# Kernel tuning notes

Hardware: AMD Instinct MI355X
Metric: run time of the kernel (lower is better)

Reference implementation:

```python
import jax, jax.numpy as jnp
import numpy as np


def setup_inputs() -> dict:
    key = jax.random.key(0)
    k1, k2 = jax.random.split(key)
    B, N, C = 2, 1024, 64  # batch_size, block_num, out_channels
    regional_means = jax.random.normal(k1, (B, N, C), dtype=jnp.float32)
    # nn.Parameter randn then kaiming_uniform_: just use scaled random weights
    W = jax.random.normal(k2, (C, C), dtype=jnp.float32) * (1.0 / np.sqrt(C))
    return {"regional_means": regional_means, "W": W, "c": C}


def reference(regional_means, W, c):
    # regional_means: (B, N, c); W: (c, c)
    B, N, _ = regional_means.shape
    M = W @ W.T  # (c, c), PSD Mahalanobis metric
    # pairwise differences diff[b, i, j] = means[b, i] - means[b, j]  -> (B, N, N, c)
    # (original materializes this via repeat/permute; sign flip from its final
    #  permute is irrelevant since the quadratic form is even)
    diff = regional_means[:, :, None, :] - regional_means[:, None, :, :]
    # quadratic form q[b,i,j] = diff^T M diff
    q = jnp.einsum('bijc,cd,bijd->bij', diff, M, diff)
    adj = jnp.exp(-q) + jnp.eye(N, dtype=regional_means.dtype)[None, :, :]
    return adj
```

## Files before the change

### kernel.cpp

```cpp
#include <hip/hip_runtime.h>
#include <hip/hip_bf16.h>
#include <math.h>


typedef __attribute__((ext_vector_type(8))) short bf16x8;
typedef __attribute__((ext_vector_type(4))) float f32x4;

#define PITCH 72

static __device__ __forceinline__ void store4bf(__hip_bfloat16* p, float4 v) {
    __hip_bfloat16 h[4] = {__float2bfloat16(v.x), __float2bfloat16(v.y),
                           __float2bfloat16(v.z), __float2bfloat16(v.w)};
    *(uint2*)p = *(const uint2*)h;
}

__global__ void __launch_bounds__(512, 4) adj_fused_mfma2(
    const float* __restrict__ X, const float* __restrict__ W,
    float* __restrict__ out, int N)
{
    __shared__ __hip_bfloat16 sX[2][64][PITCH];
    __shared__ __hip_bfloat16 sWT[64][PITCH];
    __shared__ float rs[2][64];

    const int b    = blockIdx.z;
    const int ib   = blockIdx.y << 6;
    const int jb   = blockIdx.x << 6;
    const bool diag = (ib == jb);
    const int t    = threadIdx.x;
    const int w    = t >> 6;
    const int lane = t & 63;
    const int m    = lane & 15;
    const int q    = lane >> 4;

    const float* __restrict__ Xb = X + (size_t)b * N * 64;

    const float4* W4  = (const float4*)W;
    const float4* Xi4 = (const float4*)(Xb + (size_t)ib * 64);
    const float4* Xj4 = (const float4*)(Xb + (size_t)jb * 64);
#pragma unroll
    for (int it = 0; it < 2; ++it) {
        const int idx = it * 512 + t;
        const int row = idx >> 4;
        const int c4  = (idx & 15) << 2;
        const float4 wv = W4[idx];
        sWT[c4 + 0][row] = __float2bfloat16(wv.x);
        sWT[c4 + 1][row] = __float2bfloat16(wv.y);
        sWT[c4 + 2][row] = __float2bfloat16(wv.z);
        sWT[c4 + 3][row] = __float2bfloat16(wv.w);
        store4bf(&sX[0][row][c4], Xi4[idx]);
        if (!diag) store4bf(&sX[1][row][c4], Xj4[idx]);
    }
    __syncthreads();

    {
        const int src  = w >> 2;
        const int band = (w & 3) << 4;
        if (!(diag && src)) {
            const bf16x8 a0 = *(const bf16x8*)&sX[src][band + m][q * 8];
            const bf16x8 a1 = *(const bf16x8*)&sX[src][band + m][q * 8 + 32];
            float p[4] = {0.f, 0.f, 0.f, 0.f};
#pragma unroll
            for (int ci = 0; ci < 4; ++ci) {
                const bf16x8 b0 = *(const bf16x8*)&sWT[(ci << 4) + m][q * 8];
                const bf16x8 b1 = *(const bf16x8*)&sWT[(ci << 4) + m][q * 8 + 32];
                f32x4 acc = {0.f, 0.f, 0.f, 0.f};
                acc = __builtin_amdgcn_mfma_f32_16x16x32_bf16(a0, b0, acc, 0, 0, 0);
                acc = __builtin_amdgcn_mfma_f32_16x16x32_bf16(a1, b1, acc, 0, 0, 0);
#pragma unroll
                for (int v = 0; v < 4; ++v) {
                    const __hip_bfloat16 hb = __float2bfloat16(acc[v]);
                    sX[src][band + q * 4 + v][(ci << 4) + m] = hb;
                    const float f = __bfloat162float(hb);
                    p[v] = fmaf(f, f, p[v]);
                }
            }
#pragma unroll
            for (int off = 1; off < 16; off <<= 1)
#pragma unroll
                for (int v = 0; v < 4; ++v) p[v] += __shfl_xor(p[v], off, 64);
            if (m == 0)
#pragma unroll
                for (int v = 0; v < 4; ++v) rs[src][band + q * 4 + v] = p[v];
        }
    }
    __syncthreads();

    const __hip_bfloat16 (*pYi)[PITCH] = sX[0];
    const __hip_bfloat16 (*pYj)[PITCH] = diag ? sX[0] : sX[1];
    const float* prj = diag ? rs[0] : rs[1];

    const int jband = (w & 3) << 4;
    const int ihalf = w >> 2;

    const bf16x8 ja0 = *(const bf16x8*)&pYj[jband + m][q * 8];
    const bf16x8 ja1 = *(const bf16x8*)&pYj[jband + m][q * 8 + 32];
    float rj[4];
#pragma unroll
    for (int v = 0; v < 4; ++v) rj[v] = prj[jband + (q << 2) + v];

    const size_t obase = (size_t)b * N * N;
#pragma unroll
    for (int s = 0; s < 2; ++s) {
        const int isub   = (ihalf << 1) + s;
        const int ilocal = (isub << 4) + m;
        const bf16x8 ib0 = *(const bf16x8*)&pYi[ilocal][q * 8];
        const bf16x8 ib1 = *(const bf16x8*)&pYi[ilocal][q * 8 + 32];
        f32x4 acc = {0.f, 0.f, 0.f, 0.f};
        acc = __builtin_amdgcn_mfma_f32_16x16x32_bf16(ja0, ib0, acc, 0, 0, 0);
        acc = __builtin_amdgcn_mfma_f32_16x16x32_bf16(ja1, ib1, acc, 0, 0, 0);
        const float riv = rs[0][ilocal];
        f32x4 vals;
#pragma unroll
        for (int v = 0; v < 4; ++v) {
            const float qq = riv + rj[v] - 2.f * acc[v];
            float val = __expf(-qq);
            if (diag && ilocal == jband + (q << 2) + v) val += 1.f;
            vals[v] = val;
        }
        *(f32x4*)&out[obase + (size_t)(ib + ilocal) * N + jb + jband + (q << 2)]
            = vals;
    }
}

extern "C" void kernel_launch(void* const* d_in, const int* in_sizes, int n_in,
                              void* d_out, int out_size, void* d_ws, size_t ws_size,
                              hipStream_t stream) {
    (void)n_in; (void)d_ws; (void)ws_size;
    const float* X = (const float*)d_in[0];
    const float* W = (const float*)d_in[1];
    float* out = (float*)d_out;

    const int C  = 64;
    const int BN = in_sizes[0] / C;
    const int N  = (int)(((long long)out_size * C) / in_sizes[0]);
    const int B  = BN / N;

    adj_fused_mfma2<<<dim3(N / 64, N / 64, B), 512, 0, stream>>>(X, W, out, N);
}
```

Baseline: 63.26 us.

## Precompute Y=XW and row norms once in workspace, then run gram-only kernel

Splits the fused kernel into two launches. The first computes Y = X·W (bf16) and the squared row norms once per row and writes them to the workspace buffer. The second reads Y directly from global memory to build the Gram tile and apply the exp. This removes the redundant per-tile recomputation of X·W and the shared-memory staging, at the cost of an extra launch and a dependency between the two kernels. The fused kernel remains as a fallback when the workspace is missing or too small.

```diff
diff --git a/kernel.cpp b/kernel.cpp
--- a/kernel.cpp
+++ b/kernel.cpp
@@ -12,6 +12,110 @@
     __hip_bfloat16 h[4] = {__float2bfloat16(v.x), __float2bfloat16(v.y),
                            __float2bfloat16(v.z), __float2bfloat16(v.w)};
     *(uint2*)p = *(const uint2*)h;
+}
+
+__global__ void __launch_bounds__(256, 2) compute_y(
+    const float* __restrict__ X, const float* __restrict__ W,
+    __hip_bfloat16* __restrict__ Yw, float* __restrict__ Rw)
+{
+    __shared__ __hip_bfloat16 sX[64][PITCH];
+    __shared__ __hip_bfloat16 sWT[64][PITCH];
+    const int t    = threadIdx.x;
+    const int wv   = t >> 6;
+    const int lane = t & 63;
+    const int m    = lane & 15;
+    const int q    = lane >> 4;
+    const int band = wv << 4;
+    const long long r0 = (long long)blockIdx.x << 6;
+
+    const float4* W4 = (const float4*)W;
+    const float4* X4 = (const float4*)(X + r0 * 64);
+#pragma unroll
+    for (int it = 0; it < 4; ++it) {
+        const int idx = it * 256 + t;
+        const int row = idx >> 4;
+        const int c4  = (idx & 15) << 2;
+        const float4 wv4 = W4[idx];
+        sWT[c4 + 0][row] = __float2bfloat16(wv4.x);
+        sWT[c4 + 1][row] = __float2bfloat16(wv4.y);
+        sWT[c4 + 2][row] = __float2bfloat16(wv4.z);
+        sWT[c4 + 3][row] = __float2bfloat16(wv4.w);
+        store4bf(&sX[row][c4], X4[idx]);
+    }
+    __syncthreads();
+
+    const bf16x8 a0 = *(const bf16x8*)&sX[band + m][q * 8];
+    const bf16x8 a1 = *(const bf16x8*)&sX[band + m][q * 8 + 32];
+    float p[4] = {0.f, 0.f, 0.f, 0.f};
+#pragma unroll
+    for (int ci = 0; ci < 4; ++ci) {
+        const bf16x8 b0 = *(const bf16x8*)&sWT[(ci << 4) + m][q * 8];
+        const bf16x8 b1 = *(const bf16x8*)&sWT[(ci << 4) + m][q * 8 + 32];
+        f32x4 acc = {0.f, 0.f, 0.f, 0.f};
+        acc = __builtin_amdgcn_mfma_f32_16x16x32_bf16(a0, b0, acc, 0, 0, 0);
+        acc = __builtin_amdgcn_mfma_f32_16x16x32_bf16(a1, b1, acc, 0, 0, 0);
+#pragma unroll
+        for (int v = 0; v < 4; ++v) {
+            const __hip_bfloat16 hb = __float2bfloat16(acc[v]);
+            Yw[(r0 + band + q * 4 + v) * 64 + (ci << 4) + m] = hb;
+            const float f = __bfloat162float(hb);
+            p[v] = fmaf(f, f, p[v]);
+        }
+    }
+#pragma unroll
+    for (int off = 1; off < 16; off <<= 1)
+#pragma unroll
+        for (int v = 0; v < 4; ++v) p[v] += __shfl_xor(p[v], off, 64);
+    if (m == 0)
+#pragma unroll
+        for (int v = 0; v < 4; ++v) Rw[r0 + band + q * 4 + v] = p[v];
+}
+
+__global__ void __launch_bounds__(512, 4) adj_gram(
+    const __hip_bfloat16* __restrict__ Yw, const float* __restrict__ Rw,
+    float* __restrict__ out, int N)
+{
+    const int b     = blockIdx.z;
+    const int ibase = blockIdx.y << 6;
+    const int jbase = blockIdx.x << 6;
+    const int t     = threadIdx.x;
+    const int w     = t >> 6;
+    const int lane  = t & 63;
+    const int m     = lane & 15;
+    const int q     = lane >> 4;
+    const int jband = (w & 3) << 4;
+    const int ihalf = w >> 2;
+
+    const __hip_bfloat16* __restrict__ Yb = Yw + (size_t)b * N * 64;
+    const float* __restrict__ Rb = Rw + (size_t)b * N;
+
+    const int jrow = jbase + jband + m;
+    const bf16x8 ja0 = *(const bf16x8*)&Yb[(size_t)jrow * 64 + q * 8];
+    const bf16x8 ja1 = *(const bf16x8*)&Yb[(size_t)jrow * 64 + q * 8 + 32];
+    const f32x4 rj = *(const f32x4*)&Rb[jbase + jband + (q << 2)];
+
+    const size_t obase = (size_t)b * N * N;
+#pragma unroll
+    for (int s = 0; s < 2; ++s) {
+        const int ilocal = (((ihalf << 1) + s) << 4) + m;
+        const int irow   = ibase + ilocal;
+        const bf16x8 ib0 = *(const bf16x8*)&Yb[(size_t)irow * 64 + q * 8];
+        const bf16x8 ib1 = *(const bf16x8*)&Yb[(size_t)irow * 64 + q * 8 + 32];
+        f32x4 acc = {0.f, 0.f, 0.f, 0.f};
+        acc = __builtin_amdgcn_mfma_f32_16x16x32_bf16(ja0, ib0, acc, 0, 0, 0);
+        acc = __builtin_amdgcn_mfma_f32_16x16x32_bf16(ja1, ib1, acc, 0, 0, 0);
+        const float riv  = Rb[irow];
+        const int jcol0  = jbase + jband + (q << 2);
+        f32x4 vals;
+#pragma unroll
+        for (int v = 0; v < 4; ++v) {
+            const float qq = fmaf(-2.f, acc[v], riv + rj[v]);
+            float val = __expf(-qq);
+            if (irow == jcol0 + v) val += 1.f;
+            vals[v] = val;
+        }
+        *(f32x4*)&out[obase + (size_t)irow * N + jcol0] = vals;
+    }
 }
 
 __global__ void __launch_bounds__(512, 4) adj_fused_mfma2(
@@ -33,7 +137,6 @@
     const int q    = lane >> 4;
 
     const float* __restrict__ Xb = X + (size_t)b * N * 64;
-
     const float4* W4  = (const float4*)W;
     const float4* Xi4 = (const float4*)(Xb + (size_t)ib * 64);
     const float4* Xj4 = (const float4*)(Xb + (size_t)jb * 64);
@@ -125,7 +228,7 @@
 extern "C" void kernel_launch(void* const* d_in, const int* in_sizes, int n_in,
                               void* d_out, int out_size, void* d_ws, size_t ws_size,
                               hipStream_t stream) {
-    (void)n_in; (void)d_ws; (void)ws_size;
+    (void)n_in;
     const float* X = (const float*)d_in[0];
     const float* W = (const float*)d_in[1];
     float* out = (float*)d_out;
@@ -135,5 +238,16 @@
     const int N  = (int)(((long long)out_size * C) / in_sizes[0]);
     const int B  = BN / N;
 
-    adj_fused_mfma2<<<dim3(N / 64, N / 64, B), 512, 0, stream>>>(X, W, out, N);
-}
+    const size_t ws_needed = (size_t)BN * C * sizeof(__hip_bfloat16)
+                           + (size_t)BN * sizeof(float);
+
+    if (d_ws != nullptr && ws_size >= ws_needed) {
+        __hip_bfloat16* Yw = (__hip_bfloat16*)d_ws;
+        float* Rw = (float*)((char*)d_ws
+                             + (size_t)BN * C * sizeof(__hip_bfloat16));
+        compute_y<<<BN / 64, 256, 0, stream>>>(X, W, Yw, Rw);
+        adj_gram<<<dim3(N / 64, N / 64, B), 512, 0, stream>>>(Yw, Rw, out, N);
+    } else {
+        adj_fused_mfma2<<<dim3(N / 64, N / 64, B), 512, 0, stream>>>(X, W, out, N);
+    }
+}
```

New measurement: 64.73 us. 2.3% more time.
